# Performance work log

Hardware: AMD Instinct MI355X
Metric: run time of the kernel (lower is better)

Reference implementation:

```python
import jax, jax.numpy as jnp
import numpy as np

DIM = 2048
HEADS = 32
DIM_HEAD = 64
FF_INNER = DIM * 4
SCALE_BASE = 512
FUSED = HEADS * DIM_HEAD + DIM_HEAD + DIM_HEAD + FF_INNER * 2  # 18560


def setup_inputs() -> dict:
    key = jax.random.key(0)
    k1, k2, k3, k4 = jax.random.split(key, 4)
    b, n = 2, 2048
    x = jax.random.normal(k1, (b, n, DIM), dtype=jnp.float32)
    W_fused = jax.random.normal(k2, (FUSED, DIM), dtype=jnp.float32) * 0.02
    W_attn_out = jax.random.normal(k3, (DIM, HEADS * DIM_HEAD), dtype=jnp.float32) * 0.02
    W_ff_out = jax.random.normal(k4, (DIM, FF_INNER), dtype=jnp.float32) * 0.02
    gamma = jnp.ones((DIM,), dtype=jnp.float32)
    return {"x": x, "gamma": gamma, "W_fused": W_fused,
            "W_attn_out": W_attn_out, "W_ff_out": W_ff_out}


def _rotate_half(t):
    t1, t2 = jnp.split(t, 2, axis=-1)
    return jnp.concatenate((-t2, t1), axis=-1)


def _rotary(n, dtype):
    # xpos rotary embeddings: freqs [n, dim_head], scale [n, dim_head]
    inv_freq = 1.0 / (10000.0 ** (jnp.arange(0, DIM_HEAD, 2, dtype=jnp.float32) / DIM_HEAD))
    t = jnp.arange(n, dtype=jnp.float32)
    freqs = t[:, None] * inv_freq[None, :]
    freqs = jnp.concatenate((freqs, freqs), axis=-1)
    power = (t - n // 2) / SCALE_BASE
    scale_base_vec = (jnp.arange(0, DIM_HEAD, 2, dtype=jnp.float32) + 0.4 * DIM_HEAD) / (1.4 * DIM_HEAD)
    scale = scale_base_vec[None, :] ** power[:, None]
    scale = jnp.concatenate((scale, scale), axis=-1)
    return freqs.astype(dtype), scale.astype(dtype)


def _apply_rotary(pos, t, scale):
    return t * jnp.cos(pos) * scale + _rotate_half(t) * jnp.sin(pos) * scale


def reference(x, gamma, W_fused, W_attn_out, W_ff_out):
    b, n, d = x.shape
    # LayerNorm (beta fixed at zero)
    mu = jnp.mean(x, axis=-1, keepdims=True)
    var = jnp.mean((x - mu) ** 2, axis=-1, keepdims=True)
    xn = (x - mu) * jax.lax.rsqrt(var + 1e-5) * gamma

    # fused QKV + FF projection
    proj = jnp.einsum('bnd,fd->bnf', xn, W_fused)
    attn_inner = HEADS * DIM_HEAD
    q = proj[..., :attn_inner]
    k = proj[..., attn_inner:attn_inner + DIM_HEAD]
    v = proj[..., attn_inner + DIM_HEAD:attn_inner + 2 * DIM_HEAD]
    ff = proj[..., attn_inner + 2 * DIM_HEAD:]

    # multi-query attention with xpos rotary
    q = q.reshape(b, n, HEADS, DIM_HEAD).transpose(0, 2, 1, 3)  # b h n d
    q = q * (DIM_HEAD ** -0.5)
    pos, scale = _rotary(n, x.dtype)
    q = _apply_rotary(pos, q, scale)          # broadcasts over b,h
    k = _apply_rotary(pos, k, 1.0 / scale)    # k is [b, n, dim_head]

    sim = jnp.einsum('bhid,bjd->bhij', q, k)
    causal_mask = jnp.triu(jnp.ones((n, n), dtype=bool), k=1)
    sim = jnp.where(causal_mask, -jnp.finfo(sim.dtype).max, sim)
    attn = jax.nn.softmax(sim, axis=-1)
    out = jnp.einsum('bhij,bjd->bhid', attn, v)
    out = out.transpose(0, 2, 1, 3).reshape(b, n, attn_inner)
    attn_out = jnp.einsum('bnf,df->bnd', out, W_attn_out)

    # SwiGLU FF
    ff_x, gate = jnp.split(ff, 2, axis=-1)
    ff_hidden = jax.nn.silu(gate) * ff_x
    ff_out = jnp.einsum('bnf,df->bnd', ff_hidden, W_ff_out)

    return attn_out + ff_out
```

## Files before the change

kernel.cpp:

```cpp
#include <hip/hip_runtime.h>
#include <cstdint>
#include <cstddef>

typedef __bf16 bf16;
typedef float f32x4 __attribute__((ext_vector_type(4)));
typedef bf16  bf16x4 __attribute__((ext_vector_type(4)));
typedef bf16  bf16x8 __attribute__((ext_vector_type(8)));

#define DIMD   2048
#define HEADS  32
#define DH     64
#define FFI    8192
#define FUSEDN 18560
#define FUSEDP 18688
#define BB     2
#define NN     2048
#define MROWS  4096
#define K2     10240

__device__ __forceinline__ void gl_lds16(const void* g, void* l) {
  __builtin_amdgcn_global_load_lds(
      (__attribute__((address_space(1))) void*)const_cast<void*>(g),
      (__attribute__((address_space(3))) void*)l, 16, 0, 0);
}

template <int THREADS>
__device__ __forceinline__ void stage_i(const bf16* g, long ldk,
                                        bf16* region, int instr, int tid) {
  int row = instr * (THREADS / 8) + (tid >> 3);
  int cs  = (tid & 7) ^ (row & 7);
  gl_lds16(g + (size_t)row * ldk + cs * 8,
           region + (size_t)instr * (THREADS * 8) + (size_t)(tid & ~63) * 8);
}

template <typename FA, typename FB>
__device__ __forceinline__ void gemm_2ph(FA fa, FB fb, const int NT,
    bf16* As, bf16* Bs, f32x4 (&acc)[4][4],
    const int tid, const int wrow, const int nbase, const int l15, const int h4)
{
  const char* aP[2]; const char* bP[2];
  const int arow = wrow + l15, brow = nbase + l15;
#pragma unroll
  for (int ks = 0; ks < 2; ks++) {
    aP[ks] = (const char*)As + arow * 128 + (((ks * 4 + h4) ^ (arow & 7)) * 16);
    bP[ks] = (const char*)Bs + brow * 128 + (((ks * 4 + h4) ^ (brow & 7)) * 16);
  }
  for (int t = 0; t < NT; ++t) {
    __syncthreads();
    {
      SrcT_fwd:;
      auto a = fa(t); auto b = fb(t);
#pragma unroll
      for (int q = 0; q < 4; q++) stage_i<256>(a.g, a.ldk, As, q, tid);
#pragma unroll
      for (int q = 0; q < 4; q++) stage_i<256>(b.g, b.ldk, Bs, q, tid);
    }
    __syncthreads();
#pragma unroll
    for (int ks = 0; ks < 2; ks++) {
      bf16x8 af[4], bfr[4];
#pragma unroll
      for (int m_ = 0; m_ < 4; m_++) af[m_]  = *(const bf16x8*)(aP[ks] + m_ * 2048);
#pragma unroll
      for (int n_ = 0; n_ < 4; n_++) bfr[n_] = *(const bf16x8*)(bP[ks] + n_ * 2048);
#pragma unroll
      for (int m_ = 0; m_ < 4; m_++)
#pragma unroll
        for (int n_ = 0; n_ < 4; n_++)
          acc[m_][n_] = __builtin_amdgcn_mfma_f32_16x16x32_bf16(af[m_], bfr[n_], acc[m_][n_], 0, 0, 0);
    }
  }
}

struct SrcT { const bf16* g; long ldk; };

__global__ void k_cvt_flat(const float* __restrict__ s, bf16* __restrict__ d, long total8) {
  long stride = (long)gridDim.x * blockDim.x;
  for (long i = (long)blockIdx.x * blockDim.x + threadIdx.x; i < total8; i += stride) {
    long e = i << 3;
    float4 v0 = *(const float4*)(s + e);
    float4 v1 = *(const float4*)(s + e + 4);
    bf16x8 o;
    o[0]=(bf16)v0.x; o[1]=(bf16)v0.y; o[2]=(bf16)v0.z; o[3]=(bf16)v0.w;
    o[4]=(bf16)v1.x; o[5]=(bf16)v1.y; o[6]=(bf16)v1.z; o[7]=(bf16)v1.w;
    *(bf16x8*)(d + e) = o;
  }
}

__global__ void k_cvt_str8(const float* __restrict__ s, bf16* __restrict__ d,
                           long total8, int colshift, int dstride, int doff) {
  long stride = (long)gridDim.x * blockDim.x;
  for (long i = (long)blockIdx.x * blockDim.x + threadIdx.x; i < total8; i += stride) {
    long e = i << 3;
    long r = e >> colshift;
    int  c = (int)(e & ((1L << colshift) - 1));
    float4 v0 = *(const float4*)(s + e);
    float4 v1 = *(const float4*)(s + e + 4);
    bf16x8 o;
    o[0]=(bf16)v0.x; o[1]=(bf16)v0.y; o[2]=(bf16)v0.z; o[3]=(bf16)v0.w;
    o[4]=(bf16)v1.x; o[5]=(bf16)v1.y; o[6]=(bf16)v1.z; o[7]=(bf16)v1.w;
    *(bf16x8*)(d + r * (long)dstride + doff + c) = o;
  }
}

__global__ __launch_bounds__(256) void k_ln(const float* __restrict__ x,
                                            const float* __restrict__ g,
                                            bf16* __restrict__ xn) {
  int row = blockIdx.x, t = threadIdx.x;
  const float4* xr = (const float4*)(x + (size_t)row * DIMD);
  float4 a = xr[t*2], b = xr[t*2+1];
  float s  = a.x+a.y+a.z+a.w + b.x+b.y+b.z+b.w;
  float s2 = a.x*a.x+a.y*a.y+a.z*a.z+a.w*a.w + b.x*b.x+b.y*b.y+b.z*b.z+b.w*b.w;
  for (int o = 1; o < 64; o <<= 1) { s += __shfl_xor(s, o); s2 += __shfl_xor(s2, o); }
  __shared__ float rs[8];
  if ((t & 63) == 0) { rs[t>>6] = s; rs[4 + (t>>6)] = s2; }
  __syncthreads();
  s = rs[0]+rs[1]+rs[2]+rs[3]; s2 = rs[4]+rs[5]+rs[6]+rs[7];
  float mu = s * (1.f/DIMD);
  float var = s2 * (1.f/DIMD) - mu*mu;
  float rstd = rsqrtf(var + 1e-5f);
  const float4* gr = (const float4*)g;
  float4 g0 = gr[t*2], g1 = gr[t*2+1];
  bf16x8 o;
  o[0]=(bf16)((a.x-mu)*rstd*g0.x); o[1]=(bf16)((a.y-mu)*rstd*g0.y);
  o[2]=(bf16)((a.z-mu)*rstd*g0.z); o[3]=(bf16)((a.w-mu)*rstd*g0.w);
  o[4]=(bf16)((b.x-mu)*rstd*g1.x); o[5]=(bf16)((b.y-mu)*rstd*g1.y);
  o[6]=(bf16)((b.z-mu)*rstd*g1.z); o[7]=(bf16)((b.w-mu)*rstd*g1.w);
  *(bf16x8*)(xn + (size_t)row * DIMD + t*8) = o;
}

__global__ __launch_bounds__(256, 3) void k_gemm1(const bf16* __restrict__ xn,
                                                  const bf16* __restrict__ wf,
                                                  bf16* __restrict__ q_raw,
                                                  bf16* __restrict__ k_buf,
                                                  bf16* __restrict__ v_t,
                                                  bf16* __restrict__ proj_ff) {
  __shared__ bf16 As[128*64];
  __shared__ bf16 Bs[128*64];
  const int tid = threadIdx.x, w = tid >> 6, l = tid & 63;
  const int l15 = l & 15, h4 = l >> 4;
  const int wrow = (w >> 1) * 64, nbase = (w & 1) * 64;
  const int bid = blockIdx.x;
  const int bs = (bid & 7) * 584 + (bid >> 3);
  const int mt = bs / 146, nt = bs - mt * 146;
  const int m0 = mt * 128, f0 = nt * 128;

  f32x4 acc[4][4];
#pragma unroll
  for (int i = 0; i < 4; i++)
#pragma unroll
    for (int j = 0; j < 4; j++) acc[i][j] = (f32x4){0.f,0.f,0.f,0.f};

  auto fa = [&](int t) -> SrcT { return SrcT{ xn + (size_t)m0 * DIMD + t * 64, (long)DIMD }; };
  auto fb = [&](int t) -> SrcT { return SrcT{ wf + (size_t)f0 * DIMD + t * 64, (long)DIMD }; };
  gemm_2ph(fa, fb, DIMD / 64, As, Bs, acc, tid, wrow, nbase, l15, h4);

#pragma unroll
  for (int m_ = 0; m_ < 4; m_++)
#pragma unroll
    for (int nf = 0; nf < 4; nf++) {
      int fcol = f0 + nbase + nf*16 + l15;
      if (fcol < FUSEDN) {
#pragma unroll
        for (int j = 0; j < 4; j++) {
          int m = m0 + wrow + m_*16 + h4*4 + j;
          bf16 bv = (bf16)acc[m_][nf][j];
          int b = m >> 11, n = m & 2047;
          if (fcol < 2048) {
            int hh = fcol >> 6, d = fcol & 63;
            q_raw[(((size_t)(b*HEADS + hh) * NN + n) << 6) + d] = bv;
          } else if (fcol < 2112) {
            k_buf[(((size_t)(b*NN + n)) << 6) + (fcol - 2048)] = bv;
          } else if (fcol < 2176) {
            v_t[(((size_t)(b*DH + (fcol - 2112))) << 11) + n] = bv;
          } else {
            proj_ff[((size_t)m << 14) + (fcol - 2176)] = bv;
          }
        }
      }
    }
}

__global__ __launch_bounds__(256, 3) void k_gemm2(const bf16* __restrict__ u_o,
                                                  const bf16* __restrict__ ffh,
                                                  const bf16* __restrict__ wcat,
                                                  float* __restrict__ out) {
  __shared__ bf16 As[128*64];
  __shared__ bf16 Bs[128*64];
  const int tid = threadIdx.x, w = tid >> 6, l = tid & 63;
  const int l15 = l & 15, h4 = l >> 4;
  const int wrow = (w >> 1) * 64, nbase = (w & 1) * 64;
  const int bid = blockIdx.x;
  const int bs = (bid & 7) * 64 + (bid >> 3);
  const int mt = bs >> 4, nt = bs & 15;
  const int m0 = mt * 128, f0 = nt * 128;

  f32x4 acc[4][4];
#pragma unroll
  for (int i = 0; i < 4; i++)
#pragma unroll
    for (int j = 0; j < 4; j++) acc[i][j] = (f32x4){0.f,0.f,0.f,0.f};

  auto fa = [&](int t) -> SrcT {
    if (t < 32) return SrcT{ u_o + (size_t)m0 * DIMD + t * 64, (long)DIMD };
    return SrcT{ ffh + (size_t)m0 * 16384 + (t - 32) * 64, (long)16384 };
  };
  auto fb = [&](int t) -> SrcT { return SrcT{ wcat + (size_t)f0 * K2 + t * 64, (long)K2 }; };
  gemm_2ph(fa, fb, K2 / 64, As, Bs, acc, tid, wrow, nbase, l15, h4);

#pragma unroll
  for (int m_ = 0; m_ < 4; m_++)
#pragma unroll
    for (int nf = 0; nf < 4; nf++) {
      int fcol = f0 + nbase + nf*16 + l15;
#pragma unroll
      for (int j = 0; j < 4; j++) {
        int m = m0 + wrow + m_*16 + h4*4 + j;
        out[(size_t)m * DIMD + fcol] = acc[m_][nf][j];
      }
    }
}

__global__ void k_rope(bf16* __restrict__ q_raw, bf16* __restrict__ k_buf) {
  const long QT = (long)BB*HEADS*NN*32;
  const long TOT = QT + (long)BB*NN*32;
  long gid = (long)blockIdx.x * blockDim.x + threadIdx.x;
  if (gid >= TOT) return;
  bool isq = gid < QT;
  long idx = isq ? gid : gid - QT;
  int  i = (int)(idx & 31);
  long row = idx >> 5;
  int  n = (int)(row & (NN - 1));
  bf16* base = (isq ? q_raw : k_buf) + row * DH;
  float t1 = (float)base[i];
  float t2 = (float)base[i + 32];
  float inv_freq = exp2f((float)i * -0.4152410118f);
  float th = (float)n * inv_freq;
  float sn, cs;
  __sincosf(th, &sn, &cs);
  float power = ((float)n - (float)(NN/2)) * (1.f/512.f);
  float sb = ((float)(2*i) + 25.6f) * (1.f/89.6f);
  float sc = exp2f((isq ? power : -power) * __log2f(sb));
  float mm = isq ? 0.125f : 1.0f;
  float o1 = (t1*cs - t2*sn) * sc * mm;
  float o2 = (t2*cs + t1*sn) * sc * mm;
  base[i]      = (bf16)o1;
  base[i + 32] = (bf16)o2;
}

__global__ __launch_bounds__(256) void k_attn(const bf16* __restrict__ qbuf,
                                              const bf16* __restrict__ kbuf,
                                              const bf16* __restrict__ vtb,
                                              bf16* __restrict__ uo) {
  __shared__ bf16 Qs[128*64];
  __shared__ bf16 Ks[32*64];
  __shared__ bf16 Vs[64*32];
  const int tid = threadIdx.x, w = tid >> 6, l = tid & 63;
  const int l15 = l & 15, h4 = l >> 4;
  const int bid = blockIdx.x;
  const int qt = bid & 15, bh = bid >> 4;
  const int h = bh & (HEADS - 1), b = bh >> 5;
  const int q0 = qt * 128;
  const bf16* Qg = qbuf + ((size_t)(b*HEADS + h) * NN + q0) * DH;
  const bf16* Kg = kbuf + (size_t)b * NN * DH;
  const bf16* Vg = vtb + (size_t)b * DH * NN;

#pragma unroll
  for (int c = 0; c < 4; c++) {
    int chunk = c*256 + tid;
    int r = chunk >> 3, cc = chunk & 7;
    int col8 = (cc ^ (r & 7)) << 3;
    gl_lds16(Qg + (size_t)r*DH + col8, Qs + ((size_t)(chunk & ~63) << 3));
  }
  __syncthreads();

  const int wq0 = q0 + w*32;
  bf16x8 qfr[2][2];
#pragma unroll
  for (int qf = 0; qf < 2; qf++)
#pragma unroll
    for (int c = 0; c < 2; c++) {
      int row = w*32 + qf*16 + l15;
      int x = (64*c + 16*h4) ^ (16*(row & 7));
      qfr[qf][c] = *(const bf16x8*)((const char*)Qs + row*128 + x);
    }

  f32x4 zf = {0.f,0.f,0.f,0.f};
  f32x4 o_[2][4];
#pragma unroll
  for (int qf = 0; qf < 2; qf++)
#pragma unroll
    for (int nf = 0; nf < 4; nf++) o_[qf][nf] = zf;
  float mrun[2] = {-3e38f, -3e38f};
  float lrun[2] = {0.f, 0.f};

  const int nsteps = (q0 + 128) >> 5;
  for (int kt = 0; kt < nsteps; kt++) {
    const int kv0 = kt << 5;
    {
      int r = tid >> 3, cc = tid & 7;
      int col8 = (cc ^ (r & 7)) << 3;
      gl_lds16(Kg + (size_t)(kv0 + r)*DH + col8, Ks + ((size_t)(tid & ~63) << 3));
    }
    {
      int d = tid >> 2, cc = tid & 3;
      int col8 = (cc ^ (d & 3)) << 3;
      gl_lds16(Vg + (size_t)d*NN + kv0 + col8, Vs + ((size_t)(tid & ~63) << 3));
    }
    __syncthreads();
    if (kv0 <= wq0 + 31) {
      bf16x8 ka[2][2];
#pragma unroll
      for (int kvf = 0; kvf < 2; kvf++)
#pragma unroll
        for (int c = 0; c < 2; c++) {
          int r = kvf*16 + l15;
          int x = (64*c + 16*h4) ^ (16*(r & 7));
          ka[kvf][c] = *(const bf16x8*)((const char*)Ks + r*128 + x);
        }
      f32x4 st[2][2];
#pragma unroll
      for (int kvf = 0; kvf < 2; kvf++)
#pragma unroll
        for (int qf = 0; qf < 2; qf++) {
          f32x4 s = __builtin_amdgcn_mfma_f32_16x16x32_bf16(ka[kvf][0], qfr[qf][0], zf, 0, 0, 0);
          s = __builtin_amdgcn_mfma_f32_16x16x32_bf16(ka[kvf][1], qfr[qf][1], s, 0, 0, 0);
          st[kvf][qf] = s;
        }
      if (kv0 + 31 > wq0) {
#pragma unroll
        for (int kvf = 0; kvf < 2; kvf++)
#pragma unroll
          for (int j = 0; j < 4; j++) {
            int kvg = kv0 + kvf*16 + h4*4 + j;
#pragma unroll
            for (int qf = 0; qf < 2; qf++) {
              int qg = wq0 + qf*16 + l15;
              if (kvg > qg) st[kvf][qf][j] = -3e38f;
            }
          }
      }
      bf16x8 pa[2];
#pragma unroll
      for (int qf = 0; qf < 2; qf++) {
        float vmax = -3e38f;
#pragma unroll
        for (int kvf = 0; kvf < 2; kvf++)
#pragma unroll
          for (int j = 0; j < 4; j++) vmax = fmaxf(vmax, st[kvf][qf][j]);
        vmax = fmaxf(vmax, __shfl_xor(vmax, 16));
        vmax = fmaxf(vmax, __shfl_xor(vmax, 32));
        float mnew = fmaxf(mrun[qf], vmax);
        float corr = __expf(mrun[qf] - mnew);
        float ps = 0.f;
        float pv_[8];
#pragma unroll
        for (int kvf = 0; kvf < 2; kvf++)
#pragma unroll
          for (int j = 0; j < 4; j++) {
            float p = __expf(st[kvf][qf][j] - mnew);
            pv_[kvf*4 + j] = p; ps += p;
          }
        ps += __shfl_xor(ps, 16);
        ps += __shfl_xor(ps, 32);
        lrun[qf] = lrun[qf]*corr + ps;
        mrun[qf] = mnew;
        bf16x8 t;
#pragma unroll
        for (int i = 0; i < 8; i++) t[i] = (bf16)pv_[i];
        pa[qf] = t;
#pragma unroll
        for (int j = 0; j < 4; j++) {
          float cj = __shfl(corr, (l & 48) | (h4*4 + j), 64);
#pragma unroll
          for (int nf = 0; nf < 4; nf++) o_[qf][nf][j] *= cj;
        }
      }
#pragma unroll
      for (int nf = 0; nf < 4; nf++) {
        int d_ = nf*16 + l15;
        int swz = 16*(d_ & 3);
        const char* vrow = (const char*)Vs + d_*64;
        bf16x4 v0 = *(const bf16x4*)(vrow + ((8*h4) ^ swz));
        bf16x4 v1 = *(const bf16x4*)(vrow + ((8*h4 + 32) ^ swz));
        bf16x8 vb = __builtin_shufflevector(v0, v1, 0,1,2,3,4,5,6,7);
#pragma unroll
        for (int qf = 0; qf < 2; qf++)
          o_[qf][nf] = __builtin_amdgcn_mfma_f32_16x16x32_bf16(pa[qf], vb, o_[qf][nf], 0, 0, 0);
      }
    }
    __syncthreads();
  }
#pragma unroll
  for (int qf = 0; qf < 2; qf++) {
    float inv = 1.f / lrun[qf];
#pragma unroll
    for (int j = 0; j < 4; j++) {
      float ij = __shfl(inv, (l & 48) | (h4*4 + j), 64);
      int qg = wq0 + qf*16 + h4*4 + j;
      size_t rowoff = (size_t)(b*NN + qg) * DIMD + h*DH;
#pragma unroll
      for (int nf = 0; nf < 4; nf++)
        uo[rowoff + nf*16 + l15] = (bf16)(o_[qf][nf][j] * ij);
    }
  }
}

__global__ void k_silu(bf16* __restrict__ pf) {
  const long total4 = (long)MROWS * FFI / 4;
  long stride = (long)gridDim.x * blockDim.x;
  for (long i = (long)blockIdx.x * blockDim.x + threadIdx.x; i < total4; i += stride) {
    long e = i << 2;
    long m = e >> 13;
    int  c = (int)(e & (FFI - 1));
    bf16* px = pf + (m << 14) + c;
    bf16x4 fx = *(const bf16x4*)px;
    bf16x4 gt = *(const bf16x4*)(px + FFI);
    bf16x4 r;
#pragma unroll
    for (int k = 0; k < 4; k++) {
      float g = (float)gt[k], f = (float)fx[k];
      float s = g * (1.f / (1.f + __expf(-g)));
      r[k] = (bf16)(s * f);
    }
    *(bf16x4*)px = r;
  }
}

extern "C" void kernel_launch(void* const* d_in, const int* in_sizes, int n_in,
                              void* d_out, int out_size, void* d_ws, size_t ws_size,
                              hipStream_t stream) {
  const float* x     = (const float*)d_in[0];
  const float* gamma = (const float*)d_in[1];
  const float* Wf    = (const float*)d_in[2];
  const float* Wao   = (const float*)d_in[3];
  const float* Wff   = (const float*)d_in[4];
  float* out = (float*)d_out;
  char* ws = (char*)d_ws;

  size_t o = 0;
  bf16* wfb     = (bf16*)(ws + o); o += (size_t)FUSEDP * DIMD * 2;
  bf16* wcat    = wfb;
  bf16* xn      = (bf16*)(ws + o); o += (size_t)MROWS * DIMD * 2;
  bf16* q_raw   = (bf16*)(ws + o); o += (size_t)BB*HEADS*NN*DH * 2;
  bf16* k_buf   = (bf16*)(ws + o); o += (size_t)BB*NN*DH * 2;
  bf16* v_t     = (bf16*)(ws + o); o += (size_t)BB*DH*NN * 2;
  bf16* proj_ff = (bf16*)(ws + o); o += (size_t)MROWS * 2*FFI * 2;
  bf16* u_o     = (bf16*)(ws + o); o += (size_t)MROWS * DIMD * 2;

  k_cvt_flat<<<2048, 256, 0, stream>>>(Wf, wfb, (long)FUSEDN*DIMD/8);
  k_ln<<<MROWS, 256, 0, stream>>>(x, gamma, xn);
  k_gemm1<<<(FUSEDP/128)*(MROWS/128), 256, 0, stream>>>(xn, wfb, q_raw, k_buf, v_t, proj_ff);
  k_cvt_str8<<<512,  256, 0, stream>>>(Wao, wcat, (long)DIMD*DIMD/8, 11, K2, 0);
  k_cvt_str8<<<1024, 256, 0, stream>>>(Wff, wcat, (long)DIMD*FFI/8,  13, K2, DIMD);
  {
    long tot = (long)BB*HEADS*NN*32 + (long)BB*NN*32;
    k_rope<<<(int)((tot + 255) / 256), 256, 0, stream>>>(q_raw, k_buf);
  }
  k_attn<<<BB*HEADS*(NN/128), 256, 0, stream>>>(q_raw, k_buf, v_t, u_o);
  k_silu<<<2048, 256, 0, stream>>>(proj_ff);
  k_gemm2<<<(MROWS/128)*(DIMD/128), 256, 0, stream>>>(u_o, proj_ff, wcat, out);
}
```

Before: 820.2 us.

## Split-K the output GEMM, reverse attention tile order, use nontemporal stores

The final GEMM is split into two K halves across twice as many blocks. One half writes to the output and the other to a scratch buffer that reuses the dead xn/q_raw workspace, and a new elementwise kernel adds the two. The aim is to fill more CUs than the original 512-block grid could. Attention blocks now process the heaviest causal query tiles first to balance load, and FF-projection and output stores are nontemporal. The cost is one extra launch plus a 32 MB partial write and read.

```diff
diff --git a/kernel.cpp b/kernel.cpp
--- a/kernel.cpp
+++ b/kernel.cpp
@@ -24,6 +24,11 @@
       (__attribute__((address_space(3))) void*)l, 16, 0, 0);
 }
 
+__device__ __forceinline__ void nt_store_bf16(bf16 v, bf16* p) {
+  union { bf16 b; short s; } u; u.b = v;
+  __builtin_nontemporal_store(u.s, (short*)p);
+}
+
 template <int THREADS>
 __device__ __forceinline__ void stage_i(const bf16* g, long ldk,
                                         bf16* region, int instr, int tid) {
@@ -33,6 +38,8 @@
            region + (size_t)instr * (THREADS * 8) + (size_t)(tid & ~63) * 8);
 }
 
+struct SrcT { const bf16* g; long ldk; };
+
 template <typename FA, typename FB>
 __device__ __forceinline__ void gemm_2ph(FA fa, FB fb, const int NT,
     bf16* As, bf16* Bs, f32x4 (&acc)[4][4],
@@ -48,7 +55,6 @@
   for (int t = 0; t < NT; ++t) {
     __syncthreads();
     {
-      SrcT_fwd:;
       auto a = fa(t); auto b = fb(t);
 #pragma unroll
       for (int q = 0; q < 4; q++) stage_i<256>(a.g, a.ldk, As, q, tid);
@@ -71,8 +77,6 @@
     }
   }
 }
-
-struct SrcT { const bf16* g; long ldk; };
 
 __global__ void k_cvt_flat(const float* __restrict__ s, bf16* __restrict__ d, long total8) {
   long stride = (long)gridDim.x * blockDim.x;
@@ -174,7 +178,7 @@
           } else if (fcol < 2176) {
             v_t[(((size_t)(b*DH + (fcol - 2112))) << 11) + n] = bv;
           } else {
-            proj_ff[((size_t)m << 14) + (fcol - 2176)] = bv;
+            nt_store_bf16(bv, proj_ff + ((size_t)m << 14) + (fcol - 2176));
           }
         }
       }
@@ -184,16 +188,20 @@
 __global__ __launch_bounds__(256, 3) void k_gemm2(const bf16* __restrict__ u_o,
                                                   const bf16* __restrict__ ffh,
                                                   const bf16* __restrict__ wcat,
-                                                  float* __restrict__ out) {
+                                                  float* __restrict__ out,
+                                                  float* __restrict__ part) {
   __shared__ bf16 As[128*64];
   __shared__ bf16 Bs[128*64];
   const int tid = threadIdx.x, w = tid >> 6, l = tid & 63;
   const int l15 = l & 15, h4 = l >> 4;
   const int wrow = (w >> 1) * 64, nbase = (w & 1) * 64;
   const int bid = blockIdx.x;
-  const int bs = (bid & 7) * 64 + (bid >> 3);
+  const int kk = bid >> 9;
+  const int inner = bid & 511;
+  const int bs = (inner & 7) * 64 + (inner >> 3);
   const int mt = bs >> 4, nt = bs & 15;
   const int m0 = mt * 128, f0 = nt * 128;
+  const int T0 = kk * 80;
 
   f32x4 acc[4][4];
 #pragma unroll
@@ -202,12 +210,14 @@
     for (int j = 0; j < 4; j++) acc[i][j] = (f32x4){0.f,0.f,0.f,0.f};
 
   auto fa = [&](int t) -> SrcT {
-    if (t < 32) return SrcT{ u_o + (size_t)m0 * DIMD + t * 64, (long)DIMD };
-    return SrcT{ ffh + (size_t)m0 * 16384 + (t - 32) * 64, (long)16384 };
+    int tt = t + T0;
+    if (tt < 32) return SrcT{ u_o + (size_t)m0 * DIMD + tt * 64, (long)DIMD };
+    return SrcT{ ffh + (size_t)m0 * 16384 + (tt - 32) * 64, (long)16384 };
   };
-  auto fb = [&](int t) -> SrcT { return SrcT{ wcat + (size_t)f0 * K2 + t * 64, (long)K2 }; };
-  gemm_2ph(fa, fb, K2 / 64, As, Bs, acc, tid, wrow, nbase, l15, h4);
-
+  auto fb = [&](int t) -> SrcT { return SrcT{ wcat + (size_t)f0 * K2 + (t + T0) * 64, (long)K2 }; };
+  gemm_2ph(fa, fb, 80, As, Bs, acc, tid, wrow, nbase, l15, h4);
+
+  float* dst = kk ? part : out;
 #pragma unroll
   for (int m_ = 0; m_ < 4; m_++)
 #pragma unroll
@@ -216,9 +226,20 @@
 #pragma unroll
       for (int j = 0; j < 4; j++) {
         int m = m0 + wrow + m_*16 + h4*4 + j;
-        out[(size_t)m * DIMD + fcol] = acc[m_][nf][j];
+        __builtin_nontemporal_store(acc[m_][nf][j], dst + (size_t)m * DIMD + fcol);
       }
     }
+}
+
+__global__ void k_addout(float* __restrict__ out, const float* __restrict__ part, long total4) {
+  long stride = (long)gridDim.x * blockDim.x;
+  for (long i = (long)blockIdx.x * blockDim.x + threadIdx.x; i < total4; i += stride) {
+    long e = i << 2;
+    float4 a = *(const float4*)(out + e);
+    float4 b = *(const float4*)(part + e);
+    float4 r; r.x = a.x + b.x; r.y = a.y + b.y; r.z = a.z + b.z; r.w = a.w + b.w;
+    *(float4*)(out + e) = r;
+  }
 }
 
 __global__ void k_rope(bf16* __restrict__ q_raw, bf16* __restrict__ k_buf) {
@@ -258,7 +279,8 @@
   const int tid = threadIdx.x, w = tid >> 6, l = tid & 63;
   const int l15 = l & 15, h4 = l >> 4;
   const int bid = blockIdx.x;
-  const int qt = bid & 15, bh = bid >> 4;
+  const int qt = 15 - (bid & 15);
+  const int bh = bid >> 4;
   const int h = bh & (HEADS - 1), b = bh >> 5;
   const int q0 = qt * 128;
   const bf16* Qg = qbuf + ((size_t)(b*HEADS + h) * NN + q0) * DH;
@@ -447,6 +469,7 @@
   bf16* v_t     = (bf16*)(ws + o); o += (size_t)BB*DH*NN * 2;
   bf16* proj_ff = (bf16*)(ws + o); o += (size_t)MROWS * 2*FFI * 2;
   bf16* u_o     = (bf16*)(ws + o); o += (size_t)MROWS * DIMD * 2;
+  float* part   = (float*)xn;
 
   k_cvt_flat<<<2048, 256, 0, stream>>>(Wf, wfb, (long)FUSEDN*DIMD/8);
   k_ln<<<MROWS, 256, 0, stream>>>(x, gamma, xn);
@@ -459,5 +482,6 @@
   }
   k_attn<<<BB*HEADS*(NN/128), 256, 0, stream>>>(q_raw, k_buf, v_t, u_o);
   k_silu<<<2048, 256, 0, stream>>>(proj_ff);
-  k_gemm2<<<(MROWS/128)*(DIMD/128), 256, 0, stream>>>(u_o, proj_ff, wcat, out);
-}
+  k_gemm2<<<2*(MROWS/128)*(DIMD/128), 256, 0, stream>>>(u_o, proj_ff, wcat, out, part);
+  k_addout<<<2048, 256, 0, stream>>>(out, part, (long)MROWS*DIMD/4);
+}
```

Result: slower. 852.3 us (+3.9%).
